# Kernel optimization log

Hardware: AMD Instinct MI355X
Metric: run time of the kernel (lower is better)

## Reference

```python
import jax, jax.numpy as jnp
import numpy as np

N = 16384   # must equal C**2 so the rel-pos embed broadcasts with x
C = 128     # in_channels
K = 9       # k (min legal for C=128: (2k-1)^2 >= 2C-1)
C_OUT = 256


def setup_inputs() -> dict:
    key = jax.random.key(0)
    k1, k2, k3 = jax.random.split(key, 3)
    x = jax.random.normal(k1, (N, C), dtype=jnp.float32)
    rel_pos_table = jax.random.normal(k2, ((2 * K - 1) ** 2, C), dtype=jnp.float32) * 0.02
    W = jax.random.normal(k3, (2 * C, C_OUT), dtype=jnp.float32) / np.float32(np.sqrt(2 * C))
    b = jnp.zeros((C_OUT,), dtype=jnp.float32)
    return {"x": x, "rel_pos_table": rel_pos_table, "W": W, "b": b}


def _knn_indices(x, k):
    # brute-force kNN (torch_cluster knn_graph, loop=False), dilation=1 -> no edge subsampling
    sq = jnp.sum(x * x, axis=-1)                       # [N]
    d = sq[:, None] + sq[None, :] - 2.0 * (x @ x.T)    # [N, N] squared distances
    d = d.at[jnp.diag_indices(x.shape[0])].set(jnp.inf)  # exclude self-loops
    _, idx = jax.lax.top_k(-d, k)                      # [N, k] nearest neighbors
    return idx


def reference(x, rel_pos_table, W, b):
    n, c = x.shape
    # 1) graph built on RAW x (before rel-pos add), as in the torch forward
    nbr = _knn_indices(x, K)                           # [N, K]
    # 2) learnable relative positional embedding: grid_size = x.shape[1] = C
    ar = jnp.arange(c)
    rel = (ar[:, None] - ar[None, :] + c - 1).reshape(-1)  # [C*C] == [N]
    x = x + rel_pos_table[rel]                         # [N, C]
    # 3) MRConv: max-relative aggregation + concat + 1x1 linear
    x_j = x[nbr]                                       # [N, K, C] neighbor gather
    m = jnp.max(x_j - x[:, None, :], axis=1)           # [N, C] max over neighbors
    return jnp.concatenate([x, m], axis=-1) @ W + b    # [N, C_OUT]
```

## Files before the change

### kernel.cpp

```cpp
#include <hip/hip_runtime.h>

#define NPTS 16384
#define CH 128
#define KNN 9
#define NCAND 12
#define NHALF 4
#define COUT 256
#define RG 16
#define RCAND 3

typedef __attribute__((ext_vector_type(8))) short bf16x8;
typedef __attribute__((ext_vector_type(4))) float f32x4;
typedef __attribute__((address_space(1))) const unsigned gu32;
typedef __attribute__((address_space(3))) unsigned lu32;
typedef unsigned long long u64;


__device__ __forceinline__ unsigned bfhi2(float x0, float x1) {
    unsigned u0 = __float_as_uint(x0), u1 = __float_as_uint(x1);
    unsigned r0 = (u0 + 0x7fffu + ((u0 >> 16) & 1u));
    unsigned r1 = (u1 + 0x7fffu + ((u1 >> 16) & 1u));
    return (r0 >> 16) | (r1 & 0xffff0000u);
}

__device__ __forceinline__ u64 mkkey(float d, int idx) {
    unsigned b = __float_as_uint(d);
    unsigned s = b ^ ((unsigned)((int)b >> 31) | 0x80000000u);
    return ((u64)s << 16) | (unsigned)idx;
}

struct TopK12 {
    u64 k0,k1,k2,k3,k4,k5,k6,k7,k8,k9,ka,kb;
};
struct TopK9 {
    u64 k0,k1,k2,k3,k4,k5,k6,k7,k8;
};

__device__ __forceinline__ void ins12(TopK12& T, u64 k) {
    if (k >= T.kb) return;
    bool b0 = k < T.k0;
    bool b1 = k < T.k1;
    bool b2 = k < T.k2;
    bool b3 = k < T.k3;
    bool b4 = k < T.k4;
    bool b5 = k < T.k5;
    bool b6 = k < T.k6;
    bool b7 = k < T.k7;
    bool b8 = k < T.k8;
    bool b9 = k < T.k9;
    bool ba = k < T.ka;
    T.kb = ba ? T.ka : k;
    T.ka = b9 ? T.k9 : (ba ? k : T.ka);
    T.k9 = b8 ? T.k8 : (b9 ? k : T.k9);
    T.k8 = b7 ? T.k7 : (b8 ? k : T.k8);
    T.k7 = b6 ? T.k6 : (b7 ? k : T.k7);
    T.k6 = b5 ? T.k5 : (b6 ? k : T.k6);
    T.k5 = b4 ? T.k4 : (b5 ? k : T.k5);
    T.k4 = b3 ? T.k3 : (b4 ? k : T.k4);
    T.k3 = b2 ? T.k2 : (b3 ? k : T.k3);
    T.k2 = b1 ? T.k1 : (b2 ? k : T.k2);
    T.k1 = b0 ? T.k0 : (b1 ? k : T.k1);
    T.k0 = b0 ? k : T.k0;
}

__device__ __forceinline__ void ins9(TopK9& T, u64 k) {
    if (k >= T.k8) return;
    bool b0 = k < T.k0;
    bool b1 = k < T.k1;
    bool b2 = k < T.k2;
    bool b3 = k < T.k3;
    bool b4 = k < T.k4;
    bool b5 = k < T.k5;
    bool b6 = k < T.k6;
    bool b7 = k < T.k7;
    T.k8 = b7 ? T.k7 : k;
    T.k7 = b6 ? T.k6 : (b7 ? k : T.k7);
    T.k6 = b5 ? T.k5 : (b6 ? k : T.k6);
    T.k5 = b4 ? T.k4 : (b5 ? k : T.k5);
    T.k4 = b3 ? T.k3 : (b4 ? k : T.k4);
    T.k3 = b2 ? T.k2 : (b3 ? k : T.k3);
    T.k2 = b1 ? T.k1 : (b2 ? k : T.k2);
    T.k1 = b0 ? T.k0 : (b1 ? k : T.k1);
    T.k0 = b0 ? k : T.k0;
}

__device__ __forceinline__ void merge_shfl(TopK12& T, int mask) {
    u64 o0=__shfl_xor(T.k0,mask), o1=__shfl_xor(T.k1,mask), o2=__shfl_xor(T.k2,mask);
    u64 o3=__shfl_xor(T.k3,mask), o4=__shfl_xor(T.k4,mask), o5=__shfl_xor(T.k5,mask);
    u64 o6=__shfl_xor(T.k6,mask), o7=__shfl_xor(T.k7,mask), o8=__shfl_xor(T.k8,mask);
    u64 o9=__shfl_xor(T.k9,mask), oa=__shfl_xor(T.ka,mask), ob=__shfl_xor(T.kb,mask);
    ins12(T,o0); ins12(T,o1); ins12(T,o2); ins12(T,o3);
    ins12(T,o4); ins12(T,o5); ins12(T,o6); ins12(T,o7);
    ins12(T,o8); ins12(T,o9); ins12(T,oa); ins12(T,ob);
}

__device__ __forceinline__ void merge_shfl9(TopK9& T, int mask) {
    u64 o0=__shfl_xor(T.k0,mask), o1=__shfl_xor(T.k1,mask), o2=__shfl_xor(T.k2,mask);
    u64 o3=__shfl_xor(T.k3,mask), o4=__shfl_xor(T.k4,mask), o5=__shfl_xor(T.k5,mask);
    u64 o6=__shfl_xor(T.k6,mask), o7=__shfl_xor(T.k7,mask), o8=__shfl_xor(T.k8,mask);
    ins9(T,o0); ins9(T,o1); ins9(T,o2); ins9(T,o3);
    ins9(T,o4); ins9(T,o5); ins9(T,o6); ins9(T,o7); ins9(T,o8);
}

__global__ __launch_bounds__(256) void sqnp_kernel(const float* __restrict__ x,
                                                   float* __restrict__ sq) {
    const int i = blockIdx.x * 256 + threadIdx.x;
    const float4* row4 = (const float4*)(x + (size_t)i * CH);
    float r[8];
    {
        float4 a = row4[0], b = row4[1];
        r[0] = __fmul_rn(a.x, a.x); r[1] = __fmul_rn(a.y, a.y);
        r[2] = __fmul_rn(a.z, a.z); r[3] = __fmul_rn(a.w, a.w);
        r[4] = __fmul_rn(b.x, b.x); r[5] = __fmul_rn(b.y, b.y);
        r[6] = __fmul_rn(b.z, b.z); r[7] = __fmul_rn(b.w, b.w);
    }
#pragma unroll
    for (int g = 1; g < 16; ++g) {
        float4 a = row4[2 * g], b = row4[2 * g + 1];
        r[0] = __fadd_rn(r[0], __fmul_rn(a.x, a.x));
        r[1] = __fadd_rn(r[1], __fmul_rn(a.y, a.y));
        r[2] = __fadd_rn(r[2], __fmul_rn(a.z, a.z));
        r[3] = __fadd_rn(r[3], __fmul_rn(a.w, a.w));
        r[4] = __fadd_rn(r[4], __fmul_rn(b.x, b.x));
        r[5] = __fadd_rn(r[5], __fmul_rn(b.y, b.y));
        r[6] = __fadd_rn(r[6], __fmul_rn(b.z, b.z));
        r[7] = __fadd_rn(r[7], __fmul_rn(b.w, b.w));
    }
    float t0 = __fadd_rn(__fadd_rn(r[0], r[1]), __fadd_rn(r[2], r[3]));
    float t1 = __fadd_rn(__fadd_rn(r[4], r[5]), __fadd_rn(r[6], r[7]));
    sq[i] = __fadd_rn(t0, t1);
}

__global__ __launch_bounds__(256) void split_kernel(const float* __restrict__ x,
                                                    short* __restrict__ xhi) {
    const int P = blockIdx.x * 256 + threadIdx.x;
    const int r = P >> 4;
    const int s = P & 15;
    const int phys = s ^ (r & 15);
    const float4* src = (const float4*)(x + (size_t)r * CH) + s * 2;
    float4 f0 = src[0], f1 = src[1];
    uint4 h;
    h.x = bfhi2(f0.x, f0.y);
    h.y = bfhi2(f0.z, f0.w);
    h.z = bfhi2(f1.x, f1.y);
    h.w = bfhi2(f1.z, f1.w);
    *(uint4*)&xhi[(size_t)r * 128 + phys * 8] = h;
}

__global__ __launch_bounds__(256) void wt_kernel(const float* __restrict__ W,
                                                 float* __restrict__ Wt) {
    const int c = blockIdx.x;
    const int k = threadIdx.x;
    Wt[(size_t)c * (2 * CH) + k] = W[(size_t)k * COUT + c];
}

__global__ __launch_bounds__(256, 3) void knn_kernel(const short* __restrict__ xhi,
                                                     const float* __restrict__ sq,
                                                     unsigned short* __restrict__ cand) {
    __shared__ short Bhi[2 * 64 * 128];
    const int t = threadIdx.x;
    const int row0 = blockIdx.x * 64;
    const int half = blockIdx.y;
    const int ctbeg = half * (NPTS / NHALF);
    const int ctend = ctbeg + NPTS / NHALF;

    const int lane = t & 63;
    const int w = t >> 6;
    const int m = lane & 15;
    const int quad = lane >> 4;

#pragma unroll
    for (int it = 0; it < 4; ++it) {
        const int P = t + it * 256;
        __builtin_amdgcn_global_load_lds(
            (gu32*)&xhi[(size_t)ctbeg * 128 + P * 8],
            (lu32*)&Bhi[(it * 256 + w * 64) * 8], 16, 0, 0);
    }
    const short* qrow = xhi + (size_t)(row0 + 16 * w + m) * 128;
    const bf16x8 a0 = *(const bf16x8*)&qrow[((0 * 4 + quad) ^ m) * 8];
    const bf16x8 a1 = *(const bf16x8*)&qrow[((1 * 4 + quad) ^ m) * 8];
    const bf16x8 a2 = *(const bf16x8*)&qrow[((2 * 4 + quad) ^ m) * 8];
    const bf16x8 a3 = *(const bf16x8*)&qrow[((3 * 4 + quad) ^ m) * 8];

    TopK12 T;
    T.k0=T.k1=T.k2=T.k3=T.k4=T.k5=T.k6=T.k7=T.k8=T.k9=T.ka=T.kb = ~0ULL;

    const int qglob = row0 + 16 * w + m;

    u64 qk0 = ~0ULL, qk1 = ~0ULL;
    int qn = 0;

    int boff = 0;
    for (int ct = ctbeg; ct < ctend; ct += 64) {
        __syncthreads();

        const short* Bc = Bhi + boff;
        short* Bn = Bhi + (boff ^ (64 * 128));

        const int ctn = ct + 64;
        if (ctn < ctend) {
#pragma unroll
            for (int it = 0; it < 4; ++it) {
                const int P = t + it * 256;
                __builtin_amdgcn_global_load_lds(
                    (gu32*)&xhi[(size_t)ctn * 128 + P * 8],
                    (lu32*)&Bn[(it * 256 + w * 64) * 8], 16, 0, 0);
            }
        }

        f32x4 acc0 = {0.f,0.f,0.f,0.f};
        f32x4 acc1 = {0.f,0.f,0.f,0.f};
        f32x4 acc2 = {0.f,0.f,0.f,0.f};
        f32x4 acc3 = {0.f,0.f,0.f,0.f};

#pragma unroll
        for (int kc = 0; kc < 4; ++kc) {
            const int ks = ((kc * 4 + quad) ^ m) * 8;
            const bf16x8 ah = (kc == 0) ? a0 : (kc == 1) ? a1 : (kc == 2) ? a2 : a3;
            bf16x8 bh0 = *(const bf16x8*)&Bc[(0  + m) * 128 + ks];
            bf16x8 bh1 = *(const bf16x8*)&Bc[(16 + m) * 128 + ks];
            bf16x8 bh2 = *(const bf16x8*)&Bc[(32 + m) * 128 + ks];
            bf16x8 bh3 = *(const bf16x8*)&Bc[(48 + m) * 128 + ks];
            acc0 = __builtin_amdgcn_mfma_f32_16x16x32_bf16(bh0, ah, acc0, 0, 0, 0);
            acc1 = __builtin_amdgcn_mfma_f32_16x16x32_bf16(bh1, ah, acc1, 0, 0, 0);
            acc2 = __builtin_amdgcn_mfma_f32_16x16x32_bf16(bh2, ah, acc2, 0, 0, 0);
            acc3 = __builtin_amdgcn_mfma_f32_16x16x32_bf16(bh3, ah, acc3, 0, 0, 0);
        }

#pragma unroll
        for (int cg = 0; cg < 4; ++cg) {
            const f32x4 ac = (cg == 0) ? acc0 : (cg == 1) ? acc1
                           : (cg == 2) ? acc2 : acc3;
            const float4 s4 = *(const float4*)&sq[ct + cg * 16 + quad * 4];
#pragma unroll
            for (int reg = 0; reg < 4; ++reg) {
                const float sv = (reg == 0) ? s4.x : (reg == 1) ? s4.y
                               : (reg == 2) ? s4.z : s4.w;
                const float d = __builtin_fmaf(-2.f, ac[reg], sv);
                const int cgi = ct + cg * 16 + quad * 4 + reg;
                const u64 key = mkkey(d, cgi);
                const bool pass = (key < T.kb) && (cgi != qglob);
                if (pass) {
                    if (qn >= 2) {
                        ins12(T, key);
                    } else if (qn == 0) {
                        qk0 = key;
                    } else {
                        qk1 = key;
                    }
                    ++qn;
                }
            }
        }
        if (__any(qn >= 2)) {
            ins12(T, qk0);
            ins12(T, qk1);
            qk0 = qk1 = ~0ULL;
            qn = 0;
        }
        boff ^= 64 * 128;
    }

    ins12(T, qk0);
    ins12(T, qk1);
    merge_shfl(T, 16);
    merge_shfl(T, 32);

    if (quad == 0) {
        unsigned short* cp_out = cand + (size_t)qglob * (NHALF * NCAND) + half * NCAND;
        cp_out[0]=(unsigned short)T.k0; cp_out[1]=(unsigned short)T.k1;
        cp_out[2]=(unsigned short)T.k2; cp_out[3]=(unsigned short)T.k3;
        cp_out[4]=(unsigned short)T.k4; cp_out[5]=(unsigned short)T.k5;
        cp_out[6]=(unsigned short)T.k6; cp_out[7]=(unsigned short)T.k7;
        cp_out[8]=(unsigned short)T.k8; cp_out[9]=(unsigned short)T.k9;
        cp_out[10]=(unsigned short)T.ka; cp_out[11]=(unsigned short)T.kb;
    }
}

__global__ __launch_bounds__(256) void refine_np_kernel(const float* __restrict__ x,
                                                        const float* __restrict__ sq,
                                                        const unsigned short* __restrict__ cand,
                                                        unsigned short* __restrict__ nbr) {
    const int gt = blockIdx.x * 256 + threadIdx.x;
    const int i = gt >> 4;
    const int g = gt & (RG - 1);
    const float4* X4 = (const float4*)x;
    const float sqi = sq[i];

    int ci[RCAND];
#pragma unroll
    for (int m = 0; m < RCAND; ++m)
        ci[m] = (int)cand[i * (NHALF * NCAND) + g * RCAND + m];
    float dot[RCAND];
#pragma unroll
    for (int m = 0; m < RCAND; ++m) dot[m] = 0.f;
#pragma unroll 4
    for (int c4 = 0; c4 < 32; ++c4) {
        float4 xv = X4[(size_t)i * 32 + c4];
#pragma unroll
        for (int m = 0; m < RCAND; ++m) {
            float4 nv = X4[(size_t)ci[m] * 32 + c4];
            float a = dot[m];
            a = __builtin_fmaf(xv.x, nv.x, a);
            a = __builtin_fmaf(xv.y, nv.y, a);
            a = __builtin_fmaf(xv.z, nv.z, a);
            a = __builtin_fmaf(xv.w, nv.w, a);
            dot[m] = a;
        }
    }

    TopK9 T;
    T.k0=T.k1=T.k2=T.k3=T.k4=T.k5=T.k6=T.k7=T.k8 = ~0ULL;
#pragma unroll
    for (int m = 0; m < RCAND; ++m) {
        float s = __fadd_rn(sqi, sq[ci[m]]);
        float d = __fsub_rn(s, __fmul_rn(2.0f, dot[m]));
        ins9(T, mkkey(d, ci[m]));
    }

    merge_shfl9(T, 1);
    merge_shfl9(T, 2);
    merge_shfl9(T, 4);
    merge_shfl9(T, 8);

    if (g == 0) {
        unsigned short* np = nbr + (size_t)i * KNN;
        np[0]=(unsigned short)T.k0; np[1]=(unsigned short)T.k1; np[2]=(unsigned short)T.k2;
        np[3]=(unsigned short)T.k3; np[4]=(unsigned short)T.k4; np[5]=(unsigned short)T.k5;
        np[6]=(unsigned short)T.k6; np[7]=(unsigned short)T.k7; np[8]=(unsigned short)T.k8;
    }
}

__global__ __launch_bounds__(64) void out_kernel(const float* __restrict__ x,
                                                 const float* __restrict__ tab,
                                                 const float* __restrict__ Wt,
                                                 const float* __restrict__ bias,
                                                 const unsigned short* __restrict__ nbr,
                                                 float* __restrict__ out) {
    __shared__ float cat[8][260];
    const int t = threadIdx.x;
    const int row0 = blockIdx.x * 8;
    {
        const int row = t >> 3;
        const int q = t & 7;
        const int i = row0 + row;
        const int rel_i = (i >> 7) - (i & 127) + 127;
        int nb[KNN], reln[KNN];
#pragma unroll
        for (int j = 0; j < KNN; ++j) {
            nb[j] = (int)nbr[i * KNN + j];
            reln[j] = (nb[j] >> 7) - (nb[j] & 127) + 127;
        }
        const float4* X4 = (const float4*)x;
        const float4* T4 = (const float4*)tab;
#pragma unroll
        for (int cc = 0; cc < 4; ++cc) {
            const int c4 = q * 4 + cc;
            float4 xv = X4[i * 32 + c4];
            float4 tv = T4[rel_i * 32 + c4];
            float4 xi;
            xi.x = xv.x + tv.x; xi.y = xv.y + tv.y; xi.z = xv.z + tv.z; xi.w = xv.w + tv.w;
            const float ninf = -__builtin_inff();
            float4 mx = {ninf, ninf, ninf, ninf};
#pragma unroll
            for (int j = 0; j < KNN; ++j) {
                float4 nv = X4[nb[j] * 32 + c4];
                float4 ntv = T4[reln[j] * 32 + c4];
                mx.x = fmaxf(mx.x, nv.x + ntv.x - xi.x);
                mx.y = fmaxf(mx.y, nv.y + ntv.y - xi.y);
                mx.z = fmaxf(mx.z, nv.z + ntv.z - xi.z);
                mx.w = fmaxf(mx.w, nv.w + ntv.w - xi.w);
            }
            *(float4*)&cat[row][c4 * 4] = xi;
            *(float4*)&cat[row][CH + c4 * 4] = mx;
        }
    }
    __syncthreads();

    float acc[8][4];
#pragma unroll
    for (int c = 0; c < 4; ++c) {
        const float bo = bias[t + 64 * c];
#pragma unroll
        for (int i = 0; i < 8; ++i) acc[i][c] = bo;
    }

    const float4* WT4 = (const float4*)Wt;
#pragma unroll 2
    for (int c04 = 0; c04 < 64; ++c04) {
        float4 wv0 = WT4[(size_t)(t +   0) * 64 + c04];
        float4 wv1 = WT4[(size_t)(t +  64) * 64 + c04];
        float4 wv2 = WT4[(size_t)(t + 128) * 64 + c04];
        float4 wv3 = WT4[(size_t)(t + 192) * 64 + c04];
#pragma unroll
        for (int i = 0; i < 8; ++i) {
            const float4 cv = *(const float4*)&cat[i][c04 * 4];
            acc[i][0] = fmaf(cv.x, wv0.x, acc[i][0]);
            acc[i][0] = fmaf(cv.y, wv0.y, acc[i][0]);
            acc[i][0] = fmaf(cv.z, wv0.z, acc[i][0]);
            acc[i][0] = fmaf(cv.w, wv0.w, acc[i][0]);
            acc[i][1] = fmaf(cv.x, wv1.x, acc[i][1]);
            acc[i][1] = fmaf(cv.y, wv1.y, acc[i][1]);
            acc[i][1] = fmaf(cv.z, wv1.z, acc[i][1]);
            acc[i][1] = fmaf(cv.w, wv1.w, acc[i][1]);
            acc[i][2] = fmaf(cv.x, wv2.x, acc[i][2]);
            acc[i][2] = fmaf(cv.y, wv2.y, acc[i][2]);
            acc[i][2] = fmaf(cv.z, wv2.z, acc[i][2]);
            acc[i][2] = fmaf(cv.w, wv2.w, acc[i][2]);
            acc[i][3] = fmaf(cv.x, wv3.x, acc[i][3]);
            acc[i][3] = fmaf(cv.y, wv3.y, acc[i][3]);
            acc[i][3] = fmaf(cv.z, wv3.z, acc[i][3]);
            acc[i][3] = fmaf(cv.w, wv3.w, acc[i][3]);
        }
    }

#pragma unroll
    for (int i = 0; i < 8; ++i) {
#pragma unroll
        for (int c = 0; c < 4; ++c) {
            out[(size_t)(row0 + i) * COUT + t + 64 * c] = acc[i][c];
        }
    }
}

extern "C" void kernel_launch(void* const* d_in, const int* in_sizes, int n_in,
                              void* d_out, int out_size, void* d_ws, size_t ws_size,
                              hipStream_t stream) {
    (void)in_sizes; (void)n_in; (void)out_size; (void)ws_size;
    const float* x = (const float*)d_in[0];
    const float* tab = (const float*)d_in[1];
    const float* W = (const float*)d_in[2];
    const float* b = (const float*)d_in[3];
    float* out = (float*)d_out;

    char* ws = (char*)d_ws;
    float* sq = (float*)ws;
    unsigned short* nbr = (unsigned short*)(sq + NPTS);
    float* Wt = (float*)(ws + 64 * 1024 + 288 * 1024);

    short* xhi = (short*)d_out;
    unsigned short* cand = (unsigned short*)((char*)d_out + ((size_t)NPTS * CH * 2));

    sqnp_kernel<<<NPTS / 256, 256, 0, stream>>>(x, sq);
    split_kernel<<<NPTS * 16 / 256, 256, 0, stream>>>(x, xhi);
    wt_kernel<<<COUT, 2 * CH, 0, stream>>>(W, Wt);
    knn_kernel<<<dim3(NPTS / 64, NHALF), 256, 0, stream>>>(xhi, sq, cand);
    refine_np_kernel<<<NPTS * RG / 256, 256, 0, stream>>>(x, sq, cand, nbr);
    out_kernel<<<NPTS / 8, 64, 0, stream>>>(x, tab, Wt, b, nbr, out);
}
```

Baseline: 610.3 us.

## Software-pipeline kNN tile selection behind next tile's MFMA and use float threshold

The top-k selection for each 64-candidate tile is deferred by one iteration, so it runs after the next tile's MFMAs are issued. This lets the matrix-core work overlap the scalar insertion-sort code. The squared-norm loads are hoisted ahead of the MFMAs. The 64-bit key compare is replaced by a float threshold check, refreshed only after flushes, so keys are built only for passing candidates. This costs extra live registers for the previous tile's accumulators. The stale threshold can admit more candidates, which ins12 then rejects.

```diff
diff --git a/kernel.cpp b/kernel.cpp
--- a/kernel.cpp
+++ b/kernel.cpp
@@ -27,6 +27,12 @@
     unsigned b = __float_as_uint(d);
     unsigned s = b ^ ((unsigned)((int)b >> 31) | 0x80000000u);
     return ((u64)s << 16) | (unsigned)idx;
+}
+
+__device__ __forceinline__ float kb2f(u64 kb) {
+    unsigned s = (unsigned)(kb >> 16);
+    unsigned b = s ^ (~((unsigned)((int)s >> 31)) | 0x80000000u);
+    return __uint_as_float(b);
 }
 
 struct TopK12 {
@@ -189,6 +195,49 @@
 
     u64 qk0 = ~0ULL, qk1 = ~0ULL;
     int qn = 0;
+    float thrF = __uint_as_float(0x7fffffffu);
+
+#define SELECT_TILE(P0, P1, P2, P3, S0, S1, S2, S3, CTP)                      \
+    do {                                                                      \
+        _Pragma("unroll")                                                     \
+        for (int cg = 0; cg < 4; ++cg) {                                      \
+            const f32x4 ac = (cg == 0) ? P0 : (cg == 1) ? P1                  \
+                           : (cg == 2) ? P2 : P3;                             \
+            const float4 s4v = (cg == 0) ? S0 : (cg == 1) ? S1                \
+                             : (cg == 2) ? S2 : S3;                           \
+            const int cbase = (CTP) + cg * 16 + quad * 4;                     \
+            _Pragma("unroll")                                                 \
+            for (int reg = 0; reg < 4; ++reg) {                               \
+                const float sv = (reg == 0) ? s4v.x : (reg == 1) ? s4v.y      \
+                               : (reg == 2) ? s4v.z : s4v.w;                  \
+                const float d = __builtin_fmaf(-2.f, ac[reg], sv);            \
+                const int cgi = cbase + reg;                                  \
+                const bool pass = !(d > thrF) && (cgi != qglob);              \
+                if (pass) {                                                   \
+                    const u64 key = mkkey(d, cgi);                            \
+                    if (qn >= 2) {                                            \
+                        ins12(T, key);                                        \
+                    } else if (qn == 0) {                                     \
+                        qk0 = key;                                            \
+                    } else {                                                  \
+                        qk1 = key;                                            \
+                    }                                                         \
+                    ++qn;                                                     \
+                }                                                             \
+            }                                                                 \
+        }                                                                     \
+        if (__any(qn >= 2)) {                                                 \
+            ins12(T, qk0);                                                    \
+            ins12(T, qk1);                                                    \
+            qk0 = qk1 = ~0ULL;                                                \
+            qn = 0;                                                           \
+            thrF = kb2f(T.kb);                                                \
+        }                                                                     \
+    } while (0)
+
+    f32x4 p0 = {0.f,0.f,0.f,0.f}, p1 = p0, p2 = p0, p3 = p0;
+    float4 ps0 = {0.f,0.f,0.f,0.f}, ps1 = ps0, ps2 = ps0, ps3 = ps0;
+    int ctPrev = -1;
 
     int boff = 0;
     for (int ct = ctbeg; ct < ctend; ct += 64) {
@@ -207,6 +256,11 @@
                     (lu32*)&Bn[(it * 256 + w * 64) * 8], 16, 0, 0);
             }
         }
+
+        const float4 cs0 = *(const float4*)&sq[ct +  0 + quad * 4];
+        const float4 cs1 = *(const float4*)&sq[ct + 16 + quad * 4];
+        const float4 cs2 = *(const float4*)&sq[ct + 32 + quad * 4];
+        const float4 cs3 = *(const float4*)&sq[ct + 48 + quad * 4];
 
         f32x4 acc0 = {0.f,0.f,0.f,0.f};
         f32x4 acc1 = {0.f,0.f,0.f,0.f};
@@ -227,40 +281,17 @@
             acc3 = __builtin_amdgcn_mfma_f32_16x16x32_bf16(bh3, ah, acc3, 0, 0, 0);
         }
 
-#pragma unroll
-        for (int cg = 0; cg < 4; ++cg) {
-            const f32x4 ac = (cg == 0) ? acc0 : (cg == 1) ? acc1
-                           : (cg == 2) ? acc2 : acc3;
-            const float4 s4 = *(const float4*)&sq[ct + cg * 16 + quad * 4];
-#pragma unroll
-            for (int reg = 0; reg < 4; ++reg) {
-                const float sv = (reg == 0) ? s4.x : (reg == 1) ? s4.y
-                               : (reg == 2) ? s4.z : s4.w;
-                const float d = __builtin_fmaf(-2.f, ac[reg], sv);
-                const int cgi = ct + cg * 16 + quad * 4 + reg;
-                const u64 key = mkkey(d, cgi);
-                const bool pass = (key < T.kb) && (cgi != qglob);
-                if (pass) {
-                    if (qn >= 2) {
-                        ins12(T, key);
-                    } else if (qn == 0) {
-                        qk0 = key;
-                    } else {
-                        qk1 = key;
-                    }
-                    ++qn;
-                }
-            }
-        }
-        if (__any(qn >= 2)) {
-            ins12(T, qk0);
-            ins12(T, qk1);
-            qk0 = qk1 = ~0ULL;
-            qn = 0;
-        }
+        if (ctPrev >= 0) {
+            SELECT_TILE(p0, p1, p2, p3, ps0, ps1, ps2, ps3, ctPrev);
+        }
+
+        p0 = acc0; p1 = acc1; p2 = acc2; p3 = acc3;
+        ps0 = cs0; ps1 = cs1; ps2 = cs2; ps3 = cs3;
+        ctPrev = ct;
         boff ^= 64 * 128;
     }
 
+    SELECT_TILE(p0, p1, p2, p3, ps0, ps1, ps2, ps3, ctPrev);
     ins12(T, qk0);
     ins12(T, qk1);
     merge_shfl(T, 16);
@@ -275,6 +306,7 @@
         cp_out[8]=(unsigned short)T.k8; cp_out[9]=(unsigned short)T.k9;
         cp_out[10]=(unsigned short)T.ka; cp_out[11]=(unsigned short)T.kb;
     }
+#undef SELECT_TILE
 }
 
 __global__ __launch_bounds__(256) void refine_np_kernel(const float* __restrict__ x,
```

New measurement: 670.8 us. +9.9%, slower.
